# Optimization experiments

Measured on AMD Instinct MI355X. Metric: run time of the kernel, lower is better.

Reference implementation:

```python
import jax, jax.numpy as jnp
import numpy as np

HEADS = 8
DIM_HEAD = 64
SCALE = DIM_HEAD ** (-0.5)
EPS = 1e-5


def setup_inputs() -> dict:
    key = jax.random.key(0)
    k1, k2, k3, k4 = jax.random.split(key, 4)
    b, c, t = 16, 512, 4096
    hidden = HEADS * DIM_HEAD
    x = jax.random.normal(k1, (b, c, t), dtype=jnp.float32)
    W_qkv = jax.random.normal(k2, (hidden * 3, c), dtype=jnp.float32) * (c ** -0.5)
    W_out = jax.random.normal(k3, (c, hidden), dtype=jnp.float32) * (hidden ** -0.5)
    b_out = jax.random.normal(k4, (c,), dtype=jnp.float32) * 0.02
    gn_w = jnp.ones((c,), dtype=jnp.float32)
    gn_b = jnp.zeros((c,), dtype=jnp.float32)
    return {"x": x, "W_qkv": W_qkv, "W_out": W_out, "b_out": b_out,
            "gn_w": gn_w, "gn_b": gn_b}


def reference(x, W_qkv, W_out, b_out, gn_w, gn_b):
    b, c, t = x.shape
    # 1x1 conv = channel matmul: [3*hidden, c] @ [b, c, t] -> [b, 3*hidden, t]
    qkv = jnp.einsum('oc,bct->bot', W_qkv, x)
    q, k, v = jnp.split(qkv, 3, axis=1)
    q = q.reshape(b, HEADS, DIM_HEAD, t)
    k = k.reshape(b, HEADS, DIM_HEAD, t)
    v = v.reshape(b, HEADS, DIM_HEAD, t)
    q = jax.nn.softmax(q, axis=-2) * SCALE  # softmax over feature dim
    k = jax.nn.softmax(k, axis=-1)          # softmax over time dim
    # context = k @ v^T : [b,h,dk,t] x [b,h,t,dv] -> [b,h,dk,dv]
    context = jnp.einsum('bhdt,bhet->bhde', k, v)
    # out = context^T @ q : [b,h,dv,dk] x [b,h,dk,t] -> [b,h,dv,t]
    out = jnp.einsum('bhde,bhdt->bhet', context, q)
    out = out.reshape(b, HEADS * DIM_HEAD, t)
    # output 1x1 conv with bias
    out = jnp.einsum('oc,bct->bot', W_out, out) + b_out[None, :, None]
    # GroupNorm(1, dim): normalize over (channels, time) per sample
    mean = jnp.mean(out, axis=(1, 2), keepdims=True)
    var = jnp.var(out, axis=(1, 2), keepdims=True)
    out = (out - mean) * jax.lax.rsqrt(var + EPS)
    out = out * gn_w[None, :, None] + gn_b[None, :, None]
    return out
```

## Files before the change

### kernel.cpp

```cpp
#include <hip/hip_runtime.h>
#include <stdint.h>

#define B_ 16
#define C_ 512
#define T_ 4096
#define H_ 8
#define D_ 64
#define SCALE_ 0.125f
#define EPS_ 1e-5f

using ushortT = unsigned short;
using ushort8 = __attribute__((ext_vector_type(8))) unsigned short;
using short8  = __attribute__((ext_vector_type(8))) short;
using floatx4 = __attribute__((ext_vector_type(4))) float;

__device__ __forceinline__ float bf2f(ushortT u) {
  union { unsigned int i; float f; } x; x.i = ((unsigned int)u) << 16; return x.f;
}
__device__ __forceinline__ ushortT f2bf(float f) {
  union { float f; unsigned int i; } x; x.f = f;
  unsigned int r = x.i + 0x7fffu + ((x.i >> 16) & 1u);
  return (ushortT)(r >> 16);
}

#define GLD16(gp, lp)                                                          \
  __builtin_amdgcn_global_load_lds(                                            \
      (const __attribute__((address_space(1))) unsigned int*)(gp),             \
      (__attribute__((address_space(3))) unsigned int*)(lp), 16, 0, 0)

__global__ __launch_bounds__(256) void cvt_f32_bf16(const float* __restrict__ src,
                                                    ushortT* __restrict__ dst, int n4) {
  int i = blockIdx.x * 256 + threadIdx.x;
  if (i >= n4) return;
  floatx4 v = *(const floatx4*)(src + (size_t)i * 4);
  unsigned int p0 = (unsigned int)f2bf(v[0]) | ((unsigned int)f2bf(v[1]) << 16);
  unsigned int p1 = (unsigned int)f2bf(v[2]) | ((unsigned int)f2bf(v[3]) << 16);
  *(unsigned long long*)(dst + (size_t)i * 4) =
      (unsigned long long)p0 | ((unsigned long long)p1 << 32);
}

__global__ void zero_f32(float* p, int n4) {
  int i = blockIdx.x * 256 + threadIdx.x;
  if (i < n4) ((floatx4*)p)[i] = (floatx4){0.f, 0.f, 0.f, 0.f};
}

__global__ __launch_bounds__(256) void transpose_x(const float* __restrict__ x,
                                                   ushortT* __restrict__ xT) {
  __shared__ ushortT tile[64][65];
  int b = blockIdx.z;
  int t0 = blockIdx.x * 64, c0 = blockIdx.y * 64;
  const float* xb = x + (size_t)b * C_ * T_;
  ushortT* xTb = xT + (size_t)b * T_ * C_;
  for (int i = threadIdx.x; i < 4096; i += 256) {
    int cc = i >> 6, tt = i & 63;
    tile[cc][tt] = f2bf(xb[(size_t)(c0 + cc) * T_ + t0 + tt]);
  }
  __syncthreads();
  for (int i = threadIdx.x; i < 4096; i += 256) {
    int tt = i >> 6, cc = i & 63;
    xTb[(size_t)(t0 + tt) * C_ + c0 + cc] = tile[cc][tt];
  }
}

template <int MODE>
__global__ __launch_bounds__(256) void gemm_bt(
    const ushortT* __restrict__ A, const ushortT* __restrict__ Bt,
    void* __restrict__ Cc, const float* __restrict__ bias,
    float* __restrict__ stats,
    int K, int lda, int ldb, int ldc,
    unsigned long long bsA, unsigned long long bsB, unsigned long long bsC) {
  __shared__ ushortT As[128 * 32];
  __shared__ ushortT Bs[128 * 32];
  unsigned int gx = gridDim.x, gy = gridDim.y;
  unsigned int nwg = gx * gy * gridDim.z;
  unsigned int lin = blockIdx.x + gx * (blockIdx.y + gy * blockIdx.z);
  unsigned int cpx = nwg >> 3;
  unsigned int wid = (lin & 7u) * cpx + (lin >> 3);
  unsigned int bx = wid % gx;
  unsigned int tmp = wid / gx;
  unsigned int by = tmp % gy;
  unsigned int bz = tmp / gy;

  const int b = bz;
  A += (size_t)b * bsA; Bt += (size_t)b * bsB;
  const int m0 = by * 128, n0 = bx * 128;
  const int tid = threadIdx.x;
  const int w = tid >> 6, l = tid & 63;
  const int wm = (w >> 1) * 64, wn = (w & 1) * 64;
  const int quad = l >> 4, ln = l & 15;
  floatx4 acc[4][4];
#pragma unroll
  for (int i = 0; i < 4; i++)
#pragma unroll
    for (int j = 0; j < 4; j++) acc[i][j] = (floatx4){0.f, 0.f, 0.f, 0.f};

  for (int kb = 0; kb < K; kb += 32) {
#pragma unroll
    for (int i = 0; i < 2; ++i) {
      int wci = i * 256 + (tid & 192);
      int ci  = wci + (tid & 63);
      int row = ci >> 2, col = (ci & 3) << 3;
      GLD16(&A[(size_t)(m0 + row) * lda + kb + col], &As[wci * 8]);
      GLD16(&Bt[(size_t)(n0 + row) * ldb + kb + col], &Bs[wci * 8]);
    }
    __syncthreads();
    short8 af[4], bfv[4];
#pragma unroll
    for (int i = 0; i < 4; i++) af[i] = *(const short8*)(&As[(wm + i * 16 + ln) * 32 + quad * 8]);
#pragma unroll
    for (int j = 0; j < 4; j++) bfv[j] = *(const short8*)(&Bs[(wn + j * 16 + ln) * 32 + quad * 8]);
#pragma unroll
    for (int i = 0; i < 4; i++)
#pragma unroll
      for (int j = 0; j < 4; j++)
        acc[i][j] = __builtin_amdgcn_mfma_f32_16x16x32_bf16(af[i], bfv[j], acc[i][j], 0, 0, 0);
    __syncthreads();
  }

  if constexpr (MODE == 0) {
    ushortT* Co = (ushortT*)Cc + (size_t)b * bsC;
#pragma unroll
    for (int i = 0; i < 4; i++)
#pragma unroll
      for (int r = 0; r < 4; r++) {
        int row = m0 + wm + i * 16 + quad * 4 + r;
#pragma unroll
        for (int j = 0; j < 4; j++) {
          int col = n0 + wn + j * 16 + ln;
          Co[(size_t)row * ldc + col] = f2bf(acc[i][j][r]);
        }
      }
  } else if constexpr (MODE == 1) {
    float* Co = (float*)Cc + (size_t)b * bsC;
#pragma unroll
    for (int i = 0; i < 4; i++)
#pragma unroll
      for (int r = 0; r < 4; r++) {
        int row = m0 + wm + i * 16 + quad * 4 + r;
        float bv = bias ? bias[row] : 0.f;
#pragma unroll
        for (int j = 0; j < 4; j++) {
          int col = n0 + wn + j * 16 + ln;
          Co[(size_t)row * ldc + col] = acc[i][j][r] + bv;
        }
      }
  } else if constexpr (MODE == 2) {
    ushortT* Co = (ushortT*)Cc + (size_t)b * bsC;
#pragma unroll
    for (int i = 0; i < 4; i++)
#pragma unroll
      for (int r = 0; r < 4; r++) {
        float v0 = acc[i][0][r], v1 = acc[i][1][r], v2 = acc[i][2][r], v3 = acc[i][3][r];
        float mx = fmaxf(fmaxf(v0, v1), fmaxf(v2, v3));
#pragma unroll
        for (int off = 1; off < 16; off <<= 1) mx = fmaxf(mx, __shfl_xor(mx, off));
        float e0 = expf(v0 - mx), e1 = expf(v1 - mx);
        float e2 = expf(v2 - mx), e3 = expf(v3 - mx);
        float s = (e0 + e1) + (e2 + e3);
#pragma unroll
        for (int off = 1; off < 16; off <<= 1) s += __shfl_xor(s, off);
        float inv = SCALE_ / s;
        int row = m0 + wm + i * 16 + quad * 4 + r;
        size_t base = (size_t)row * ldc + n0 + wn + ln;
        Co[base +  0] = f2bf(e0 * inv);
        Co[base + 16] = f2bf(e1 * inv);
        Co[base + 32] = f2bf(e2 * inv);
        Co[base + 48] = f2bf(e3 * inv);
      }
  } else {
    float* Co = (float*)Cc + (size_t)b * bsC;
    float s = 0.f, ss = 0.f;
#pragma unroll
    for (int i = 0; i < 4; i++)
#pragma unroll
      for (int r = 0; r < 4; r++) {
        int row = m0 + wm + i * 16 + quad * 4 + r;
        float bv = bias ? bias[row] : 0.f;
#pragma unroll
        for (int j = 0; j < 4; j++) {
          int col = n0 + wn + j * 16 + ln;
          float v = acc[i][j][r] + bv;
          Co[(size_t)row * ldc + col] = v;
          s += v; ss += v * v;
        }
      }
#pragma unroll
    for (int off = 1; off < 64; off <<= 1) {
      s += __shfl_xor(s, off);
      ss += __shfl_xor(ss, off);
    }
    __shared__ float rs[4], rss[4];
    if (l == 0) { rs[w] = s; rss[w] = ss; }
    __syncthreads();
    if (tid == 0) {
      atomicAdd(&stats[b * 2],     rs[0] + rs[1] + rs[2] + rs[3]);
      atomicAdd(&stats[b * 2 + 1], rss[0] + rss[1] + rss[2] + rss[3]);
    }
  }
}

__global__ __launch_bounds__(64) void context_kv(const ushortT* __restrict__ kv,
                                                 float* __restrict__ ksum,
                                                 float* __restrict__ ct) {
  __shared__ ushortT Vs[64 * 32];
  __shared__ ushortT Ks[64 * 32];
  const int slice = blockIdx.x, h = blockIdx.y, b = blockIdx.z;
  const int t0 = slice * 512;
  const ushortT* vrow = kv + ((size_t)b * 1024 + 512 + h * 64) * T_;
  const ushortT* krow = kv + ((size_t)b * 1024 + h * 64) * T_;
  const int tid = threadIdx.x, quad = tid >> 4, ln = tid & 15;
  float rsum[4] = {0.f, 0.f, 0.f, 0.f};
  floatx4 acc[4][4];
#pragma unroll
  for (int i = 0; i < 4; i++)
#pragma unroll
    for (int j = 0; j < 4; j++) acc[i][j] = (floatx4){0.f, 0.f, 0.f, 0.f};
  for (int kb = 0; kb < 512; kb += 32) {
#pragma unroll
    for (int i = 0; i < 4; ++i) {
      int ci = i * 64 + tid;
      int row = ci >> 2, col = (ci & 3) << 3;
      GLD16(&vrow[(size_t)row * T_ + t0 + kb + col], &Vs[i * 512]);
    }
#pragma unroll
    for (int i = 0; i < 4; ++i) {
      int ci = i * 64 + tid;
      int row = ci >> 2, col = (ci & 3) << 3;
      ushort8 kr = *(const ushort8*)(&krow[(size_t)row * T_ + t0 + kb + col]);
      ushort8 ko;
      float ls = 0.f;
#pragma unroll
      for (int j = 0; j < 8; j++) {
        float e = expf(bf2f(kr[j]));
        ko[j] = f2bf(e);
        ls += e;
      }
      rsum[i] += ls;
      *(ushort8*)(&Ks[row * 32 + col]) = ko;
    }
    __syncthreads();
    short8 af[4], bfv[4];
#pragma unroll
    for (int i = 0; i < 4; i++) af[i] = *(const short8*)(&Vs[(i * 16 + ln) * 32 + quad * 8]);
#pragma unroll
    for (int j = 0; j < 4; j++) bfv[j] = *(const short8*)(&Ks[(j * 16 + ln) * 32 + quad * 8]);
#pragma unroll
    for (int i = 0; i < 4; i++)
#pragma unroll
      for (int j = 0; j < 4; j++)
        acc[i][j] = __builtin_amdgcn_mfma_f32_16x16x32_bf16(af[i], bfv[j], acc[i][j], 0, 0, 0);
    __syncthreads();
  }
  float* ks = ksum + (size_t)b * 512 + h * 64;
#pragma unroll
  for (int i = 0; i < 4; ++i) {
    float s = rsum[i];
    s += __shfl_xor(s, 1);
    s += __shfl_xor(s, 2);
    if ((tid & 3) == 0) atomicAdd(&ks[i * 16 + (tid >> 2)], s);
  }
  float* ctbh = ct + (size_t)(b * 8 + h) * 4096;
#pragma unroll
  for (int i = 0; i < 4; i++)
#pragma unroll
    for (int r = 0; r < 4; r++) {
      int e = i * 16 + quad * 4 + r;
#pragma unroll
      for (int j = 0; j < 4; j++) {
        int d = j * 16 + ln;
        atomicAdd(&ctbh[e * 64 + d], acc[i][j][r]);
      }
    }
}

__global__ __launch_bounds__(64) void ct_combine(const ushortT* __restrict__ Wobf,
                                                 const float* __restrict__ ct,
                                                 const float* __restrict__ ksum,
                                                 ushortT* __restrict__ W2) {
  __shared__ ushortT As[64 * 64];
  __shared__ float Cs[64 * 64];
  const int c0 = blockIdx.x * 64, h = blockIdx.y, b = blockIdx.z;
  const int tid = threadIdx.x, quad = tid >> 4, ln = tid & 15;
  const float* ctbh = ct + (size_t)(b * 8 + h) * 4096;
#pragma unroll
  for (int i = 0; i < 8; ++i) {
    int ci = i * 64 + tid;
    int row = ci >> 3, col = (ci & 7) << 3;
    *(uint4*)(&As[row * 64 + col]) = *(const uint4*)(&Wobf[(size_t)(c0 + row) * 512 + h * 64 + col]);
  }
#pragma unroll
  for (int i = 0; i < 16; ++i) {
    int off = (i * 64 + tid) * 4;
    *(floatx4*)(&Cs[off]) = *(const floatx4*)(&ctbh[off]);
  }
  const float* ks = ksum + (size_t)b * 512 + h * 64;
  float invd[4];
#pragma unroll
  for (int j = 0; j < 4; j++) invd[j] = 1.f / ks[j * 16 + ln];
  __syncthreads();
  floatx4 acc[4][4];
#pragma unroll
  for (int i = 0; i < 4; i++)
#pragma unroll
    for (int j = 0; j < 4; j++) acc[i][j] = (floatx4){0.f, 0.f, 0.f, 0.f};
#pragma unroll
  for (int kk = 0; kk < 2; ++kk) {
    short8 af[4], bfv[4];
#pragma unroll
    for (int i = 0; i < 4; i++) af[i] = *(const short8*)(&As[(i * 16 + ln) * 64 + kk * 32 + quad * 8]);
#pragma unroll
    for (int j = 0; j < 4; j++) {
#pragma unroll
      for (int e2 = 0; e2 < 8; ++e2)
        bfv[j][e2] = (short)f2bf(Cs[(kk * 32 + quad * 8 + e2) * 64 + j * 16 + ln] * invd[j]);
    }
#pragma unroll
    for (int i = 0; i < 4; i++)
#pragma unroll
      for (int j = 0; j < 4; j++)
        acc[i][j] = __builtin_amdgcn_mfma_f32_16x16x32_bf16(af[i], bfv[j], acc[i][j], 0, 0, 0);
  }
  ushortT* W2b = W2 + (size_t)b * 512 * 512;
#pragma unroll
  for (int i = 0; i < 4; i++)
#pragma unroll
    for (int r = 0; r < 4; r++) {
      int row = c0 + i * 16 + quad * 4 + r;
#pragma unroll
      for (int j = 0; j < 4; j++) {
        int col = h * 64 + j * 16 + ln;
        W2b[(size_t)row * 512 + col] = f2bf(acc[i][j][r]);
      }
    }
}

__global__ __launch_bounds__(256) void gn_apply(float* __restrict__ out,
                                                const float* __restrict__ stats,
                                                const float* __restrict__ gnw,
                                                const float* __restrict__ gnb) {
  int b = blockIdx.y;
  int i = blockIdx.x * 256 + threadIdx.x;
  const float invN = 1.f / (float)(C_ * T_);
  float mean = stats[b * 2] * invN;
  float var = stats[b * 2 + 1] * invN - mean * mean;
  float inv = rsqrtf(var + EPS_);
  int c = i >> 9;
  float wv = gnw[c] * inv, bv = gnb[c];
  float* p = out + (size_t)b * C_ * T_ + (size_t)i * 8;
  floatx4 v0 = *(const floatx4*)p;
  floatx4 v1 = *(const floatx4*)(p + 4);
#pragma unroll
  for (int j = 0; j < 4; j++) v0[j] = (v0[j] - mean) * wv + bv;
#pragma unroll
  for (int j = 0; j < 4; j++) v1[j] = (v1[j] - mean) * wv + bv;
  *(floatx4*)p = v0;
  *(floatx4*)(p + 4) = v1;
}

extern "C" void kernel_launch(void* const* d_in, const int* in_sizes, int n_in,
                              void* d_out, int out_size, void* d_ws, size_t ws_size,
                              hipStream_t stream) {
  (void)in_sizes; (void)n_in; (void)out_size; (void)ws_size;
  const float* x    = (const float*)d_in[0];
  const float* Wqkv = (const float*)d_in[1];
  const float* Wout = (const float*)d_in[2];
  const float* bout = (const float*)d_in[3];
  const float* gnw  = (const float*)d_in[4];
  const float* gnb  = (const float*)d_in[5];
  float* out = (float*)d_out;

  char* ws = (char*)d_ws;
  ushortT* xT   = (ushortT*)(ws);
  ushortT* qT   = (ushortT*)(ws + 67108864);
  ushortT* Wqbf = (ushortT*)(ws + 134217728);
  ushortT* Wobf = (ushortT*)(ws + 135790592);
  float*   ct   = (float*)(ws + 136314880);
  float* stats  = (float*)(ws + 138412032);
  float* ksum   = (float*)(ws);
  ushortT* W2   = (ushortT*)(ws + 1048576);
  ushortT* kv   = (ushortT*)d_out;

  cvt_f32_bf16<<<768, 256, 0, stream>>>(Wqkv, Wqbf, 196608);
  cvt_f32_bf16<<<256, 256, 0, stream>>>(Wout, Wobf, 65536);
  zero_f32<<<513, 256, 0, stream>>>(ct, 131080);

  transpose_x<<<dim3(64, 8, 16), 256, 0, stream>>>(x, xT);

  gemm_bt<0><<<dim3(32, 8, 16), 256, 0, stream>>>(
      Wqbf + 512 * 512, xT, kv, nullptr, nullptr, 512, 512, 512, 4096,
      0ULL, (unsigned long long)(T_ * 512), (unsigned long long)(1024 * T_));

  gemm_bt<2><<<dim3(4, 32, 16), 256, 0, stream>>>(
      xT, Wqbf, qT, nullptr, nullptr, 512, 512, 512, 512,
      (unsigned long long)(T_ * 512), 0ULL, (unsigned long long)(T_ * 512));

  zero_f32<<<8, 256, 0, stream>>>(ksum, 2048);

  context_kv<<<dim3(8, 8, 16), 64, 0, stream>>>(kv, ksum, ct);

  ct_combine<<<dim3(8, 8, 16), 64, 0, stream>>>(Wobf, ct, ksum, W2);

  gemm_bt<3><<<dim3(32, 4, 16), 256, 0, stream>>>(
      W2, qT, out, bout, stats, 512, 512, 512, 4096,
      (unsigned long long)(512 * 512), (unsigned long long)(T_ * 512),
      (unsigned long long)(512 * T_));

  gn_apply<<<dim3(1024, 16), 256, 0, stream>>>(out, stats, gnw, gnb);
}
```

Before: 587.4 us.

## Fuse Q and KV projections into one GEMM with exp and softmax epilogues

Replaces the two separate projection GEMMs with a single gemm_qkv launch covering all 1536 output rows. The Q tiles apply the feature-dim softmax in the epilogue and write transposed through swizzled LDS, and the K tiles apply exp before storing. context_kv now loads pre-exponentiated K directly with async loads, sums it from the fragments, and uses twice as many time slices. This removes one launch, the re-read of xT, and the exp work inside the context kernel. In exchange it stores exp(k) without max subtraction, which could overflow for large logits, and doubles the number of atomic adds into ct.

```diff
diff --git a/kernel.cpp b/kernel.cpp
--- a/kernel.cpp
+++ b/kernel.cpp
@@ -59,6 +59,132 @@
   for (int i = threadIdx.x; i < 4096; i += 256) {
     int tt = i >> 6, cc = i & 63;
     xTb[(size_t)(t0 + tt) * C_ + c0 + cc] = tile[cc][tt];
+  }
+}
+
+__global__ __launch_bounds__(256) void gemm_qkv(
+    const ushortT* __restrict__ A,
+    const ushortT* __restrict__ Bt,
+    ushortT* __restrict__ qT,
+    ushortT* __restrict__ kvout) {
+  __shared__ ushortT lds[2 * 128 * 32];
+  ushortT* As = lds;
+  ushortT* Bs = lds + 128 * 32;
+  unsigned int gx = gridDim.x, gy = gridDim.y;
+  unsigned int nwg = gx * gy * gridDim.z;
+  unsigned int lin = blockIdx.x + gx * (blockIdx.y + gy * blockIdx.z);
+  unsigned int cpx = nwg >> 3;
+  unsigned int wid = (lin & 7u) * cpx + (lin >> 3);
+  unsigned int bx = wid % gx;
+  unsigned int tmp = wid / gx;
+  unsigned int by = tmp % gy;
+  unsigned int bz = tmp / gy;
+
+  const int b = bz;
+  const ushortT* Bb = Bt + (size_t)b * (T_ * 512);
+  const int m0 = by * 128, n0 = bx * 128;
+  const int tid = threadIdx.x;
+  const int w = tid >> 6, l = tid & 63;
+  const int wm = (w >> 1) * 64, wn = (w & 1) * 64;
+  const int quad = l >> 4, ln = l & 15;
+  floatx4 acc[4][4];
+#pragma unroll
+  for (int i = 0; i < 4; i++)
+#pragma unroll
+    for (int j = 0; j < 4; j++) acc[i][j] = (floatx4){0.f, 0.f, 0.f, 0.f};
+
+  for (int kb = 0; kb < 512; kb += 32) {
+#pragma unroll
+    for (int i = 0; i < 2; ++i) {
+      int wci = i * 256 + (tid & 192);
+      int ci  = wci + (tid & 63);
+      int row = ci >> 2, col = (ci & 3) << 3;
+      GLD16(&A[(size_t)(m0 + row) * 512 + kb + col], &As[wci * 8]);
+      GLD16(&Bb[(size_t)(n0 + row) * 512 + kb + col], &Bs[wci * 8]);
+    }
+    __syncthreads();
+    short8 af[4], bfv[4];
+#pragma unroll
+    for (int i = 0; i < 4; i++) af[i] = *(const short8*)(&As[(wm + i * 16 + ln) * 32 + quad * 8]);
+#pragma unroll
+    for (int j = 0; j < 4; j++) bfv[j] = *(const short8*)(&Bs[(wn + j * 16 + ln) * 32 + quad * 8]);
+#pragma unroll
+    for (int i = 0; i < 4; i++)
+#pragma unroll
+      for (int j = 0; j < 4; j++)
+        acc[i][j] = __builtin_amdgcn_mfma_f32_16x16x32_bf16(af[i], bfv[j], acc[i][j], 0, 0, 0);
+    __syncthreads();
+  }
+
+  if (m0 < 512) {
+#pragma unroll
+    for (int j = 0; j < 4; j++) {
+      float mx = -1e30f;
+#pragma unroll
+      for (int i = 0; i < 4; i++)
+#pragma unroll
+        for (int r = 0; r < 4; r++) mx = fmaxf(mx, acc[i][j][r]);
+      mx = fmaxf(mx, __shfl_xor(mx, 16));
+      mx = fmaxf(mx, __shfl_xor(mx, 32));
+      float s = 0.f;
+#pragma unroll
+      for (int i = 0; i < 4; i++)
+#pragma unroll
+        for (int r = 0; r < 4; r++) {
+          float e = expf(acc[i][j][r] - mx);
+          acc[i][j][r] = e;
+          s += e;
+        }
+      s += __shfl_xor(s, 16);
+      s += __shfl_xor(s, 32);
+      float inv = SCALE_ / s;
+#pragma unroll
+      for (int i = 0; i < 4; i++)
+#pragma unroll
+        for (int r = 0; r < 4; r++) acc[i][j][r] *= inv;
+    }
+    ushortT* qb = qT + (size_t)b * T_ * 512;
+#pragma unroll
+    for (int half = 0; half < 2; ++half) {
+      __syncthreads();
+      if ((w >> 1) == half) {
+#pragma unroll
+        for (int i = 0; i < 4; i++)
+#pragma unroll
+          for (int r = 0; r < 4; r++) {
+            int o = i * 16 + quad * 4 + r;
+#pragma unroll
+            for (int j = 0; j < 4; j++) {
+              int t = wn + j * 16 + ln;
+              lds[t * 64 + (o ^ ((t & 7) << 3))] = f2bf(acc[i][j][r]);
+            }
+          }
+      }
+      __syncthreads();
+      int tt = tid >> 1;
+#pragma unroll
+      for (int c = 0; c < 4; ++c) {
+        int g = (tid & 1) * 4 + c;
+        short8 v = *(const short8*)(&lds[tt * 64 + ((g ^ (tt & 7)) * 8)]);
+        *(short8*)(&qb[(size_t)(n0 + tt) * 512 + m0 + half * 64 + g * 8]) = v;
+      }
+    }
+  } else {
+    const int isk = (m0 < 1024);
+    ushortT* kvb = kvout + (size_t)b * (1024 * (size_t)T_);
+#pragma unroll
+    for (int i = 0; i < 4; i++)
+#pragma unroll
+      for (int r = 0; r < 4; r++) {
+        int orow = m0 - 512 + wm + i * 16 + quad * 4 + r;
+#pragma unroll
+        for (int j = 0; j < 4; j++) {
+          int col = n0 + wn + j * 16 + ln;
+          float v = acc[i][j][r];
+          if (isk) v = expf(v);
+          kvb[(size_t)orow * T_ + col] = f2bf(v);
+        }
+      }
   }
 }
 
@@ -117,57 +243,7 @@
     __syncthreads();
   }
 
-  if constexpr (MODE == 0) {
-    ushortT* Co = (ushortT*)Cc + (size_t)b * bsC;
-#pragma unroll
-    for (int i = 0; i < 4; i++)
-#pragma unroll
-      for (int r = 0; r < 4; r++) {
-        int row = m0 + wm + i * 16 + quad * 4 + r;
-#pragma unroll
-        for (int j = 0; j < 4; j++) {
-          int col = n0 + wn + j * 16 + ln;
-          Co[(size_t)row * ldc + col] = f2bf(acc[i][j][r]);
-        }
-      }
-  } else if constexpr (MODE == 1) {
-    float* Co = (float*)Cc + (size_t)b * bsC;
-#pragma unroll
-    for (int i = 0; i < 4; i++)
-#pragma unroll
-      for (int r = 0; r < 4; r++) {
-        int row = m0 + wm + i * 16 + quad * 4 + r;
-        float bv = bias ? bias[row] : 0.f;
-#pragma unroll
-        for (int j = 0; j < 4; j++) {
-          int col = n0 + wn + j * 16 + ln;
-          Co[(size_t)row * ldc + col] = acc[i][j][r] + bv;
-        }
-      }
-  } else if constexpr (MODE == 2) {
-    ushortT* Co = (ushortT*)Cc + (size_t)b * bsC;
-#pragma unroll
-    for (int i = 0; i < 4; i++)
-#pragma unroll
-      for (int r = 0; r < 4; r++) {
-        float v0 = acc[i][0][r], v1 = acc[i][1][r], v2 = acc[i][2][r], v3 = acc[i][3][r];
-        float mx = fmaxf(fmaxf(v0, v1), fmaxf(v2, v3));
-#pragma unroll
-        for (int off = 1; off < 16; off <<= 1) mx = fmaxf(mx, __shfl_xor(mx, off));
-        float e0 = expf(v0 - mx), e1 = expf(v1 - mx);
-        float e2 = expf(v2 - mx), e3 = expf(v3 - mx);
-        float s = (e0 + e1) + (e2 + e3);
-#pragma unroll
-        for (int off = 1; off < 16; off <<= 1) s += __shfl_xor(s, off);
-        float inv = SCALE_ / s;
-        int row = m0 + wm + i * 16 + quad * 4 + r;
-        size_t base = (size_t)row * ldc + n0 + wn + ln;
-        Co[base +  0] = f2bf(e0 * inv);
-        Co[base + 16] = f2bf(e1 * inv);
-        Co[base + 32] = f2bf(e2 * inv);
-        Co[base + 48] = f2bf(e3 * inv);
-      }
-  } else {
+  {
     float* Co = (float*)Cc + (size_t)b * bsC;
     float s = 0.f, ss = 0.f;
 #pragma unroll
@@ -205,7 +281,7 @@
   __shared__ ushortT Vs[64 * 32];
   __shared__ ushortT Ks[64 * 32];
   const int slice = blockIdx.x, h = blockIdx.y, b = blockIdx.z;
-  const int t0 = slice * 512;
+  const int t0 = slice * 256;
   const ushortT* vrow = kv + ((size_t)b * 1024 + 512 + h * 64) * T_;
   const ushortT* krow = kv + ((size_t)b * 1024 + h * 64) * T_;
   const int tid = threadIdx.x, quad = tid >> 4, ln = tid & 15;
@@ -215,35 +291,24 @@
   for (int i = 0; i < 4; i++)
 #pragma unroll
     for (int j = 0; j < 4; j++) acc[i][j] = (floatx4){0.f, 0.f, 0.f, 0.f};
-  for (int kb = 0; kb < 512; kb += 32) {
+  for (int kb = 0; kb < 256; kb += 32) {
 #pragma unroll
     for (int i = 0; i < 4; ++i) {
       int ci = i * 64 + tid;
       int row = ci >> 2, col = (ci & 3) << 3;
       GLD16(&vrow[(size_t)row * T_ + t0 + kb + col], &Vs[i * 512]);
-    }
-#pragma unroll
-    for (int i = 0; i < 4; ++i) {
-      int ci = i * 64 + tid;
-      int row = ci >> 2, col = (ci & 3) << 3;
-      ushort8 kr = *(const ushort8*)(&krow[(size_t)row * T_ + t0 + kb + col]);
-      ushort8 ko;
-      float ls = 0.f;
-#pragma unroll
-      for (int j = 0; j < 8; j++) {
-        float e = expf(bf2f(kr[j]));
-        ko[j] = f2bf(e);
-        ls += e;
-      }
-      rsum[i] += ls;
-      *(ushort8*)(&Ks[row * 32 + col]) = ko;
+      GLD16(&krow[(size_t)row * T_ + t0 + kb + col], &Ks[i * 512]);
     }
     __syncthreads();
     short8 af[4], bfv[4];
 #pragma unroll
     for (int i = 0; i < 4; i++) af[i] = *(const short8*)(&Vs[(i * 16 + ln) * 32 + quad * 8]);
 #pragma unroll
-    for (int j = 0; j < 4; j++) bfv[j] = *(const short8*)(&Ks[(j * 16 + ln) * 32 + quad * 8]);
+    for (int j = 0; j < 4; j++) {
+      bfv[j] = *(const short8*)(&Ks[(j * 16 + ln) * 32 + quad * 8]);
+#pragma unroll
+      for (int e = 0; e < 8; e++) rsum[j] += bf2f((ushortT)bfv[j][e]);
+    }
 #pragma unroll
     for (int i = 0; i < 4; i++)
 #pragma unroll
@@ -253,11 +318,11 @@
   }
   float* ks = ksum + (size_t)b * 512 + h * 64;
 #pragma unroll
-  for (int i = 0; i < 4; ++i) {
-    float s = rsum[i];
-    s += __shfl_xor(s, 1);
-    s += __shfl_xor(s, 2);
-    if ((tid & 3) == 0) atomicAdd(&ks[i * 16 + (tid >> 2)], s);
+  for (int j = 0; j < 4; ++j) {
+    float s = rsum[j];
+    s += __shfl_xor(s, 16);
+    s += __shfl_xor(s, 32);
+    if (quad == 0) atomicAdd(&ks[j * 16 + ln], s);
   }
   float* ctbh = ct + (size_t)(b * 8 + h) * 4096;
 #pragma unroll
@@ -386,17 +451,11 @@
 
   transpose_x<<<dim3(64, 8, 16), 256, 0, stream>>>(x, xT);
 
-  gemm_bt<0><<<dim3(32, 8, 16), 256, 0, stream>>>(
-      Wqbf + 512 * 512, xT, kv, nullptr, nullptr, 512, 512, 512, 4096,
-      0ULL, (unsigned long long)(T_ * 512), (unsigned long long)(1024 * T_));
-
-  gemm_bt<2><<<dim3(4, 32, 16), 256, 0, stream>>>(
-      xT, Wqbf, qT, nullptr, nullptr, 512, 512, 512, 512,
-      (unsigned long long)(T_ * 512), 0ULL, (unsigned long long)(T_ * 512));
+  gemm_qkv<<<dim3(32, 12, 16), 256, 0, stream>>>(Wqbf, xT, qT, kv);
 
   zero_f32<<<8, 256, 0, stream>>>(ksum, 2048);
 
-  context_kv<<<dim3(8, 8, 16), 64, 0, stream>>>(kv, ksum, ct);
+  context_kv<<<dim3(16, 8, 16), 64, 0, stream>>>(kv, ksum, ct);
 
   ct_combine<<<dim3(8, 8, 16), 64, 0, stream>>>(Wobf, ct, ksum, W2);
 
```

Result: slower. 614.1 us (+4.6%).

## Fuse exp of K into QKV GEMM epilogue and split context over more blocks

Applied to the files above, without the earlier changes.

Moves the exponential on the K rows into the output stage of the K/V projection GEMM, so context_kv can load K directly into shared memory with async copies instead of computing exp per element. The K row sums are now taken from the bf16-rounded exp values read out of shared memory. The context kernel's time slice is halved and its grid doubled to raise parallelism, at the cost of twice as many atomic adds into ct. Unused MODE 0/1 epilogues are removed. Softmax stability still relies on skipping the max subtraction, as the code before already did.

```diff
diff --git a/kernel.cpp b/kernel.cpp
--- a/kernel.cpp
+++ b/kernel.cpp
@@ -117,7 +117,8 @@
     __syncthreads();
   }
 
-  if constexpr (MODE == 0) {
+  if constexpr (MODE == 4) {
+    const bool isk = (m0 < 512);
     ushortT* Co = (ushortT*)Cc + (size_t)b * bsC;
 #pragma unroll
     for (int i = 0; i < 4; i++)
@@ -127,21 +128,9 @@
 #pragma unroll
         for (int j = 0; j < 4; j++) {
           int col = n0 + wn + j * 16 + ln;
-          Co[(size_t)row * ldc + col] = f2bf(acc[i][j][r]);
-        }
-      }
-  } else if constexpr (MODE == 1) {
-    float* Co = (float*)Cc + (size_t)b * bsC;
-#pragma unroll
-    for (int i = 0; i < 4; i++)
-#pragma unroll
-      for (int r = 0; r < 4; r++) {
-        int row = m0 + wm + i * 16 + quad * 4 + r;
-        float bv = bias ? bias[row] : 0.f;
-#pragma unroll
-        for (int j = 0; j < 4; j++) {
-          int col = n0 + wn + j * 16 + ln;
-          Co[(size_t)row * ldc + col] = acc[i][j][r] + bv;
+          float v = acc[i][j][r];
+          if (isk) v = expf(v);
+          Co[(size_t)row * ldc + col] = f2bf(v);
         }
       }
   } else if constexpr (MODE == 2) {
@@ -205,7 +194,7 @@
   __shared__ ushortT Vs[64 * 32];
   __shared__ ushortT Ks[64 * 32];
   const int slice = blockIdx.x, h = blockIdx.y, b = blockIdx.z;
-  const int t0 = slice * 512;
+  const int t0 = slice * 256;
   const ushortT* vrow = kv + ((size_t)b * 1024 + 512 + h * 64) * T_;
   const ushortT* krow = kv + ((size_t)b * 1024 + h * 64) * T_;
   const int tid = threadIdx.x, quad = tid >> 4, ln = tid & 15;
@@ -215,35 +204,24 @@
   for (int i = 0; i < 4; i++)
 #pragma unroll
     for (int j = 0; j < 4; j++) acc[i][j] = (floatx4){0.f, 0.f, 0.f, 0.f};
-  for (int kb = 0; kb < 512; kb += 32) {
+  for (int kb = 0; kb < 256; kb += 32) {
 #pragma unroll
     for (int i = 0; i < 4; ++i) {
       int ci = i * 64 + tid;
       int row = ci >> 2, col = (ci & 3) << 3;
       GLD16(&vrow[(size_t)row * T_ + t0 + kb + col], &Vs[i * 512]);
-    }
-#pragma unroll
-    for (int i = 0; i < 4; ++i) {
-      int ci = i * 64 + tid;
-      int row = ci >> 2, col = (ci & 3) << 3;
-      ushort8 kr = *(const ushort8*)(&krow[(size_t)row * T_ + t0 + kb + col]);
-      ushort8 ko;
-      float ls = 0.f;
-#pragma unroll
-      for (int j = 0; j < 8; j++) {
-        float e = expf(bf2f(kr[j]));
-        ko[j] = f2bf(e);
-        ls += e;
-      }
-      rsum[i] += ls;
-      *(ushort8*)(&Ks[row * 32 + col]) = ko;
+      GLD16(&krow[(size_t)row * T_ + t0 + kb + col], &Ks[i * 512]);
     }
     __syncthreads();
     short8 af[4], bfv[4];
 #pragma unroll
     for (int i = 0; i < 4; i++) af[i] = *(const short8*)(&Vs[(i * 16 + ln) * 32 + quad * 8]);
 #pragma unroll
-    for (int j = 0; j < 4; j++) bfv[j] = *(const short8*)(&Ks[(j * 16 + ln) * 32 + quad * 8]);
+    for (int j = 0; j < 4; j++) {
+      bfv[j] = *(const short8*)(&Ks[(j * 16 + ln) * 32 + quad * 8]);
+#pragma unroll
+      for (int e = 0; e < 8; e++) rsum[j] += bf2f((ushortT)bfv[j][e]);
+    }
 #pragma unroll
     for (int i = 0; i < 4; i++)
 #pragma unroll
@@ -253,11 +231,11 @@
   }
   float* ks = ksum + (size_t)b * 512 + h * 64;
 #pragma unroll
-  for (int i = 0; i < 4; ++i) {
-    float s = rsum[i];
-    s += __shfl_xor(s, 1);
-    s += __shfl_xor(s, 2);
-    if ((tid & 3) == 0) atomicAdd(&ks[i * 16 + (tid >> 2)], s);
+  for (int j = 0; j < 4; ++j) {
+    float s = rsum[j];
+    s += __shfl_xor(s, 16);
+    s += __shfl_xor(s, 32);
+    if (quad == 0) atomicAdd(&ks[j * 16 + ln], s);
   }
   float* ctbh = ct + (size_t)(b * 8 + h) * 4096;
 #pragma unroll
@@ -386,7 +364,7 @@
 
   transpose_x<<<dim3(64, 8, 16), 256, 0, stream>>>(x, xT);
 
-  gemm_bt<0><<<dim3(32, 8, 16), 256, 0, stream>>>(
+  gemm_bt<4><<<dim3(32, 8, 16), 256, 0, stream>>>(
       Wqbf + 512 * 512, xT, kv, nullptr, nullptr, 512, 512, 512, 4096,
       0ULL, (unsigned long long)(T_ * 512), (unsigned long long)(1024 * T_));
 
@@ -396,7 +374,7 @@
 
   zero_f32<<<8, 256, 0, stream>>>(ksum, 2048);
 
-  context_kv<<<dim3(8, 8, 16), 64, 0, stream>>>(kv, ksum, ct);
+  context_kv<<<dim3(16, 8, 16), 64, 0, stream>>>(kv, ksum, ct);
 
   ct_combine<<<dim3(8, 8, 16), 64, 0, stream>>>(Wobf, ct, ksum, W2);
 
```

Measured after the change: 597.6 us. Within noise of the previous version (+1.7%).
